# Optimization experiments

Measured on AMD Instinct MI355X. Metric: run time of the kernel, lower is better.

Reference implementation:

```python
import jax, jax.numpy as jnp
import numpy as np

D, H, HS, L, V, B, T = 384, 8, 48, 8, 32000, 32, 128
EPS = 1e-5


def setup_inputs() -> dict:
    key = jax.random.key(0)
    ks = jax.random.split(key, 10)
    s = 0.02
    return {
        'index': jax.random.randint(ks[0], (B, T), 0, V),
        'tok_emb': jax.random.normal(ks[1], (V, D), jnp.float32) * s,
        'pos_emb': jax.random.normal(ks[2], (V, D), jnp.float32) * s,
        'Wq': jax.random.normal(ks[3], (L, D, D), jnp.float32) * s,
        'Wk': jax.random.normal(ks[4], (L, D, D), jnp.float32) * s,
        'Wv': jax.random.normal(ks[5], (L, D, D), jnp.float32) * s,
        'Wo': jax.random.normal(ks[6], (L, D, D), jnp.float32) * s,
        'bo': jnp.zeros((L, D), jnp.float32),
        'W1': jax.random.normal(ks[7], (L, D, 4 * D), jnp.float32) * s,
        'b1': jnp.zeros((L, 4 * D), jnp.float32),
        'W2': jax.random.normal(ks[8], (L, 4 * D, D), jnp.float32) * s,
        'b2': jnp.zeros((L, D), jnp.float32),
        'ln1g': jnp.ones((L, D), jnp.float32),
        'ln1b': jnp.zeros((L, D), jnp.float32),
        'ln2g': jnp.ones((L, D), jnp.float32),
        'ln2b': jnp.zeros((L, D), jnp.float32),
        'lnfg': jnp.ones((D,), jnp.float32),
        'lnfb': jnp.zeros((D,), jnp.float32),
        'lmW': jax.random.normal(ks[9], (D, V), jnp.float32) * s,
        'lmb': jnp.zeros((V,), jnp.float32),
    }


def _layer_norm(x, g, b):
    m = jnp.mean(x, axis=-1, keepdims=True)
    xc = x - m
    v = jnp.mean(xc * xc, axis=-1, keepdims=True)
    return xc * jax.lax.rsqrt(v + EPS) * g + b


def _forward(index, tok_emb, pos_emb, Wq, Wk, Wv, Wo, bo, W1, b1, W2, b2,
             ln1g, ln1b, ln2g, ln2b, lnfg, lnfb, lmW, lmb):
    Bx, Tx = index.shape
    x = tok_emb[index] + pos_emb[jnp.arange(Tx)]  # [B,T,D]
    tril = jnp.tril(jnp.ones((Tx, Tx), bool))
    scale = HS ** -0.5
    neg_inf = jnp.finfo(x.dtype).min
    for l in range(L):
        q = (x @ Wq[l]).reshape(Bx, Tx, H, HS)
        k = (x @ Wk[l]).reshape(Bx, Tx, H, HS)
        v = (x @ Wv[l]).reshape(Bx, Tx, H, HS)
        wei = jnp.einsum('bthd,bshd->bhts', q, k) * scale  # [B,H,T,T]
        wei = jnp.where(tril, wei, neg_inf)
        wei = jax.nn.softmax(wei, axis=-1)
        attn = jnp.einsum('bhts,bshd->bthd', wei, v).reshape(Bx, Tx, D)
        y = attn @ Wo[l] + bo[l]
        x = _layer_norm(x + y, ln1g[l], ln1b[l])  # post-LN as in source
        y = jax.nn.relu(x @ W1[l] + b1[l]) @ W2[l] + b2[l]
        x = _layer_norm(x + y, ln2g[l], ln2b[l])
    x = _layer_norm(x, lnfg, lnfb)
    logits = x @ lmW + lmb  # [B,T,V]
    return logits


def reference(index, tok_emb, pos_emb, Wq, Wk, Wv, Wo, bo, W1, b1, W2, b2,
              ln1g, ln1b, ln2g, ln2b, lnfg, lnfb, lmW, lmb):
    return _forward(index, tok_emb, pos_emb, Wq, Wk, Wv, Wo, bo, W1, b1, W2,
                    b2, ln1g, ln1b, ln2g, ln2b, lnfg, lnfb, lmW, lmb)
```

## Files before the change

### kernel.cpp

```cpp
#include <hip/hip_runtime.h>
#include <cstdint>
#include <cstddef>

#define D_  384
#define H_  8
#define HS_ 48
#define L_  8
#define V_  32000
#define B_  32
#define T_  128
#define M_  4096

typedef __bf16 bf16;
typedef __bf16 bf16x8 __attribute__((ext_vector_type(8)));
typedef float  floatx4 __attribute__((ext_vector_type(4)));

__device__ __forceinline__ unsigned short bfbits(float f) {
  union { bf16 b; unsigned short u; } cv; cv.b = (bf16)f; return cv.u;
}
__device__ __forceinline__ float bflo(unsigned u) {
  union { float f; unsigned x; } c; c.x = u << 16; return c.f;
}
__device__ __forceinline__ float bfhi(unsigned u) {
  union { float f; unsigned x; } c; c.x = u & 0xffff0000u; return c.f;
}

__device__ __forceinline__ float waveReduceSum(float v) {
  #pragma unroll
  for (int off = 32; off > 0; off >>= 1) v += __shfl_xor(v, off, 64);
  return v;
}

__global__ void embed_kernel(const int* __restrict__ idx, const float* __restrict__ tok,
                             const float* __restrict__ pos, float* __restrict__ x,
                             bf16* __restrict__ xb) {
  int e = blockIdx.x * 256 + threadIdx.x;
  int row = e / 96, c4 = (e % 96) * 4;
  int t = row & (T_ - 1);
  int tk = idx[row];
  const float4 tv = *(const float4*)(tok + (size_t)tk * D_ + c4);
  const float4 pv = *(const float4*)(pos + (size_t)t * D_ + c4);
  float4 o; o.x = tv.x + pv.x; o.y = tv.y + pv.y; o.z = tv.z + pv.z; o.w = tv.w + pv.w;
  *(float4*)(x + (size_t)row * D_ + c4) = o;
  uint2 u;
  u.x = (unsigned)bfbits(o.x) | ((unsigned)bfbits(o.y) << 16);
  u.y = (unsigned)bfbits(o.z) | ((unsigned)bfbits(o.w) << 16);
  *(uint2*)(xb + (size_t)row * D_ + c4) = u;
}

__device__ __forceinline__ void transpose_tile(const float* __restrict__ src, bf16* __restrict__ dst,
                                               int K, int N, int k0, int n0) {
  __shared__ float tile[32][33];
  const int r = threadIdx.x >> 5, c = threadIdx.x & 31;
  #pragma unroll
  for (int i = 0; i < 4; i++)
    tile[r + 8*i][c] = src[(size_t)(k0 + r + 8*i) * N + n0 + c];
  __syncthreads();
  #pragma unroll
  for (int i = 0; i < 4; i++)
    dst[(size_t)(n0 + r + 8*i) * K + k0 + c] = (bf16)tile[c][r + 8*i];
}

__global__ __launch_bounds__(256) void t_layer_kernel(
    const float* __restrict__ Wq, const float* __restrict__ Wk,
    const float* __restrict__ Wv, const float* __restrict__ Wo,
    const float* __restrict__ W1, const float* __restrict__ W2,
    bf16* __restrict__ wqkvoT, bf16* __restrict__ w1t, bf16* __restrict__ w2t) {
  if (blockIdx.z == 0) {
    const int mm = blockIdx.x / 12, nx = blockIdx.x % 12;
    const float* src = mm == 0 ? Wq : mm == 1 ? Wk : mm == 2 ? Wv : Wo;
    transpose_tile(src, wqkvoT + (size_t)mm * (D_ * D_), D_, D_, blockIdx.y * 32, nx * 32);
  } else if (blockIdx.z == 1) {
    transpose_tile(W1, w1t, D_, 4 * D_, blockIdx.y * 32, blockIdx.x * 32);
  } else {
    transpose_tile(W2, w2t, 4 * D_, D_, blockIdx.x * 32, blockIdx.y * 32);
  }
}

__global__ __launch_bounds__(256) void t_head_kernel(const float* __restrict__ lmW, bf16* __restrict__ dst) {
  transpose_tile(lmW, dst, D_, V_, blockIdx.y * 32, blockIdx.x * 32);
}

template<bool BIAS, bool RESID, bool RELU, bool OUTBF>
__device__ __forceinline__ void gemm_core(
    const bf16* __restrict__ A, const bf16* __restrict__ Bt,
    const float* __restrict__ bias, const float* __restrict__ resid,
    void* __restrict__ Cout, int N, int K, int m0, int n0)
{
  __shared__ bf16 As[128][56];
  __shared__ bf16 Bs[128][56];
  const int tid  = threadIdx.x;
  const int lane = tid & 63;
  const int wave = tid >> 6;
  const int wr = wave >> 1, wc = wave & 1;
  const int lrow = lane & 15, quad = lane >> 4;

  floatx4 acc[4][4];
  #pragma unroll
  for (int i = 0; i < 4; i++)
    #pragma unroll
    for (int j = 0; j < 4; j++) acc[i][j] = floatx4{0.f, 0.f, 0.f, 0.f};

  const int r0 = tid >> 2,          p0 = (tid & 3) * 8;
  const int r1 = (tid + 256) >> 2,  p1 = p0;

  for (int k0 = 0; k0 < K; k0 += 32) {
    __syncthreads();
    const uint4 a0 = *(const uint4*)(A  + (size_t)(m0 + r0) * K + k0 + p0);
    const uint4 a1 = *(const uint4*)(A  + (size_t)(m0 + r1) * K + k0 + p1);
    const uint4 b0 = *(const uint4*)(Bt + (size_t)(n0 + r0) * K + k0 + p0);
    const uint4 b1 = *(const uint4*)(Bt + (size_t)(n0 + r1) * K + k0 + p1);
    *(uint4*)&As[r0][p0] = a0;
    *(uint4*)&As[r1][p1] = a1;
    *(uint4*)&Bs[r0][p0] = b0;
    *(uint4*)&Bs[r1][p1] = b1;
    __syncthreads();
    bf16x8 af[4], bfr[4];
    #pragma unroll
    for (int mt = 0; mt < 4; mt++) af[mt]  = *(const bf16x8*)&As[wr*64 + mt*16 + lrow][quad*8];
    #pragma unroll
    for (int nt = 0; nt < 4; nt++) bfr[nt] = *(const bf16x8*)&Bs[wc*64 + nt*16 + lrow][quad*8];
    #pragma unroll
    for (int mt = 0; mt < 4; mt++)
      #pragma unroll
      for (int nt = 0; nt < 4; nt++)
        acc[mt][nt] = __builtin_amdgcn_mfma_f32_16x16x32_bf16(af[mt], bfr[nt], acc[mt][nt], 0, 0, 0);
  }

  #pragma unroll
  for (int mt = 0; mt < 4; mt++) {
    #pragma unroll
    for (int nt = 0; nt < 4; nt++) {
      const int col = n0 + wc*64 + nt*16 + lrow;
      float bv = 0.f;
      if (BIAS) bv = bias[col];
      #pragma unroll
      for (int i = 0; i < 4; i++) {
        const int row = m0 + wr*64 + mt*16 + quad*4 + i;
        float vv = acc[mt][nt][i] + bv;
        if (RESID) vv += resid[(size_t)row * N + col];
        if (RELU)  vv = vv > 0.f ? vv : 0.f;
        if (OUTBF) ((bf16*)Cout)[(size_t)row * N + col] = (bf16)vv;
        else       ((float*)Cout)[(size_t)row * N + col] = vv;
      }
    }
  }
}

template<bool BIAS, bool RESID, bool RELU, bool OUTBF>
__global__ __launch_bounds__(256) void gemm_kernel(const bf16* __restrict__ A, const bf16* __restrict__ Bt,
    const float* __restrict__ bias, const float* __restrict__ resid, void* __restrict__ C, int N, int K) {
  gemm_core<BIAS, RESID, RELU, OUTBF>(A, Bt, bias, resid, C, N, K, blockIdx.x * 128, blockIdx.y * 128);
}

__global__ __launch_bounds__(256) void gemm_qkv_kernel(const bf16* __restrict__ A, const bf16* __restrict__ Wt,
    bf16* __restrict__ q, bf16* __restrict__ k, bf16* __restrict__ v) {
  const bf16* Bt = Wt + (size_t)blockIdx.z * (D_ * D_);
  bf16* C = blockIdx.z == 0 ? q : (blockIdx.z == 1 ? k : v);
  gemm_core<false, false, false, true>(A, Bt, nullptr, nullptr, C, D_, D_, blockIdx.x * 128, blockIdx.y * 128);
}

__global__ __launch_bounds__(512) void attn_kernel(const bf16* __restrict__ q,
    const bf16* __restrict__ k, const bf16* __restrict__ v, bf16* __restrict__ attnb) {
  __shared__ float ks[T_][48];
  __shared__ float vs[T_][48];
  const int bh = blockIdx.x;
  const int b = bh >> 3, h = bh & 7;
  const int r  = threadIdx.x >> 2;
  const int qq = threadIdx.x & 3;
  const int o  = qq * 12;
  const size_t rowbase = ((size_t)(b * T_ + r)) * D_ + h * HS_ + o;
  float qr[12];
  #pragma unroll
  for (int j = 0; j < 3; j++) {
    const uint2 tk = *(const uint2*)(k + rowbase + 4*j);
    const uint2 tv = *(const uint2*)(v + rowbase + 4*j);
    const uint2 tq = *(const uint2*)(q + rowbase + 4*j);
    float4 fk, fv;
    fk.x = bflo(tk.x); fk.y = bfhi(tk.x); fk.z = bflo(tk.y); fk.w = bfhi(tk.y);
    fv.x = bflo(tv.x); fv.y = bfhi(tv.x); fv.z = bflo(tv.y); fv.w = bfhi(tv.y);
    *(float4*)&ks[r][o + 4*j] = fk;
    *(float4*)&vs[r][o + 4*j] = fv;
    qr[4*j]   = bflo(tq.x); qr[4*j+1] = bfhi(tq.x);
    qr[4*j+2] = bflo(tq.y); qr[4*j+3] = bfhi(tq.y);
  }
  __syncthreads();
  float m = -3.0e38f, l = 0.f, acc[12];
  #pragma unroll
  for (int j = 0; j < 12; j++) acc[j] = 0.f;
  const float scale = 0.14433756729740643f;
  for (int c = 0; c < T_; c++) {
    float s = 0.f;
    #pragma unroll
    for (int j = 0; j < 12; j++) s += qr[j] * ks[c][o + j];
    s += __shfl_xor(s, 1, 64);
    s += __shfl_xor(s, 2, 64);
    s *= scale;
    if (c > r) s = -3.0e38f;
    const float mn = fmaxf(m, s);
    const float al = __expf(m - mn);
    const float pp = __expf(s - mn);
    l = l * al + pp;
    #pragma unroll
    for (int j = 0; j < 12; j++) acc[j] = acc[j] * al + pp * vs[c][o + j];
    m = mn;
  }
  const float inv = 1.f / l;
  unsigned ob[6];
  #pragma unroll
  for (int j = 0; j < 6; j++)
    ob[j] = (unsigned)bfbits(acc[2*j] * inv) | ((unsigned)bfbits(acc[2*j+1] * inv) << 16);
  bf16* dst = attnb + rowbase;
  #pragma unroll
  for (int j = 0; j < 3; j++) {
    uint2 u; u.x = ob[2*j]; u.y = ob[2*j+1];
    *(uint2*)(dst + 4*j) = u;
  }
}

__global__ __launch_bounds__(256) void ln_kernel(const float* __restrict__ in,
    const float* __restrict__ g, const float* __restrict__ bta,
    float* __restrict__ xo, bf16* __restrict__ xbo) {
  const int wave = threadIdx.x >> 6, lane = threadIdx.x & 63;
  const int row = blockIdx.x * 4 + wave;
  const float* p = in + (size_t)row * D_;
  float v[6];
  #pragma unroll
  for (int j = 0; j < 6; j++) v[j] = p[lane + 64*j];
  float s = 0.f;
  #pragma unroll
  for (int j = 0; j < 6; j++) s += v[j];
  s = waveReduceSum(s);
  const float mean = s * (1.f / 384.f);
  float qv = 0.f;
  #pragma unroll
  for (int j = 0; j < 6; j++) { v[j] -= mean; qv += v[j] * v[j]; }
  qv = waveReduceSum(qv);
  const float rs = rsqrtf(qv * (1.f / 384.f) + 1e-5f);
  #pragma unroll
  for (int j = 0; j < 6; j++) {
    const int c = lane + 64*j;
    const float o = v[j] * rs * g[c] + bta[c];
    xo[(size_t)row * D_ + c]  = o;
    xbo[(size_t)row * D_ + c] = (bf16)o;
  }
}

extern "C" void kernel_launch(void* const* d_in, const int* in_sizes, int n_in,
                              void* d_out, int out_size, void* d_ws, size_t ws_size,
                              hipStream_t stream) {
  const int*   index = (const int*)  d_in[0];
  const float* tok   = (const float*)d_in[1];
  const float* pos   = (const float*)d_in[2];
  const float* Wq    = (const float*)d_in[3];
  const float* Wk    = (const float*)d_in[4];
  const float* Wv    = (const float*)d_in[5];
  const float* Wo    = (const float*)d_in[6];
  const float* bo    = (const float*)d_in[7];
  const float* W1    = (const float*)d_in[8];
  const float* b1    = (const float*)d_in[9];
  const float* W2    = (const float*)d_in[10];
  const float* b2    = (const float*)d_in[11];
  const float* ln1g  = (const float*)d_in[12];
  const float* ln1b  = (const float*)d_in[13];
  const float* ln2g  = (const float*)d_in[14];
  const float* ln2b  = (const float*)d_in[15];
  const float* lnfg  = (const float*)d_in[16];
  const float* lnfb  = (const float*)d_in[17];
  const float* lmW   = (const float*)d_in[18];
  const float* lmb   = (const float*)d_in[19];
  float* out = (float*)d_out;
  char* ws = (char*)d_ws;

  float* x     = (float*)(ws + 0);
  float* tmp   = (float*)(ws + 6291456);
  bf16*  xb    = (bf16*) (ws + 12582912);
  bf16*  qb    = (bf16*) (ws + 15728640);
  bf16*  kb    = (bf16*) (ws + 18874368);
  bf16*  vb    = (bf16*) (ws + 22020096);
  bf16*  attnb = (bf16*) (ws + 25165824);
  bf16*  hb    = (bf16*) (ws + 28311552);
  bf16*  wqkvoT= (bf16*) (ws + 40894464);
  bf16*  w1t   = (bf16*) (ws + 42074112);
  bf16*  w2t   = (bf16*) (ws + 43253760);
  bf16*  lmT   = (bf16*) (ws + 15728640);

  embed_kernel<<<1536, 256, 0, stream>>>(index, tok, pos, x, xb);
  for (int l = 0; l < L_; l++) {
    t_layer_kernel<<<dim3(48, 12, 3), 256, 0, stream>>>(
        Wq + (size_t)l * D_ * D_, Wk + (size_t)l * D_ * D_,
        Wv + (size_t)l * D_ * D_, Wo + (size_t)l * D_ * D_,
        W1 + (size_t)l * D_ * 4 * D_, W2 + (size_t)l * 4 * D_ * D_,
        wqkvoT, w1t, w2t);
    gemm_qkv_kernel<<<dim3(32, 3, 3), 256, 0, stream>>>(xb, wqkvoT, qb, kb, vb);
    attn_kernel<<<256, 512, 0, stream>>>(qb, kb, vb, attnb);
    gemm_kernel<true, true, false, false><<<dim3(32, 3), 256, 0, stream>>>(
        attnb, wqkvoT + 3 * D_ * D_, bo + l * D_, x, tmp, D_, D_);
    ln_kernel<<<1024, 256, 0, stream>>>(tmp, ln1g + l * D_, ln1b + l * D_, x, xb);
    gemm_kernel<true, false, true, true><<<dim3(32, 12), 256, 0, stream>>>(
        xb, w1t, b1 + l * 4 * D_, nullptr, hb, 4 * D_, D_);
    gemm_kernel<true, true, false, false><<<dim3(32, 3), 256, 0, stream>>>(
        hb, w2t, b2 + l * D_, x, tmp, D_, 4 * D_);
    ln_kernel<<<1024, 256, 0, stream>>>(tmp, ln2g + l * D_, ln2b + l * D_, x, xb);
  }
  ln_kernel<<<1024, 256, 0, stream>>>(x, lnfg, lnfb, x, xb);
  t_head_kernel<<<dim3(1000, 12), 256, 0, stream>>>(lmW, lmT);
  gemm_kernel<true, false, false, false><<<dim3(32, 250), 256, 0, stream>>>(
      xb, lmT, lmb, nullptr, out, V_, D_);
}
```

Measured before the change: 1.799 ms.

## Use direct global-to-LDS loads with XOR swizzle and 64-row tiles for N=384 GEMMs

The GEMM core now loads A and B tiles straight from global memory into LDS with global_load_lds, skipping the register round-trip. The LDS tiles drop their padding and use an XOR-swizzled column layout to avoid bank conflicts. The block M size becomes a template parameter, and the Wo and W2 projections switch to 64-row tiles so their launches have twice as many blocks. The main loop still uses two barriers per k-step and no double buffering, so load latency is not overlapped with the MFMA work.

```diff
diff --git a/kernel.cpp b/kernel.cpp
--- a/kernel.cpp
+++ b/kernel.cpp
@@ -29,6 +29,12 @@
   #pragma unroll
   for (int off = 32; off > 0; off >>= 1) v += __shfl_xor(v, off, 64);
   return v;
+}
+
+__device__ __forceinline__ void gload_lds16(const void* g, void* l) {
+  __builtin_amdgcn_global_load_lds(
+      (const __attribute__((address_space(1))) void*)g,
+      (__attribute__((address_space(3))) void*)l, 16, 0, 0);
 }
 
 __global__ void embed_kernel(const int* __restrict__ idx, const float* __restrict__ tok,
@@ -81,62 +87,69 @@
   transpose_tile(lmW, dst, D_, V_, blockIdx.y * 32, blockIdx.x * 32);
 }
 
-template<bool BIAS, bool RESID, bool RELU, bool OUTBF>
+template<int BM, bool BIAS, bool RESID, bool RELU, bool OUTBF>
 __device__ __forceinline__ void gemm_core(
     const bf16* __restrict__ A, const bf16* __restrict__ Bt,
     const float* __restrict__ bias, const float* __restrict__ resid,
     void* __restrict__ Cout, int N, int K, int m0, int n0)
 {
-  __shared__ bf16 As[128][56];
-  __shared__ bf16 Bs[128][56];
+  constexpr int MTC = BM / 32;
+  __shared__ bf16 As[BM * 32];
+  __shared__ bf16 Bs[128 * 32];
   const int tid  = threadIdx.x;
   const int lane = tid & 63;
   const int wave = tid >> 6;
   const int wr = wave >> 1, wc = wave & 1;
   const int lrow = lane & 15, quad = lane >> 4;
-
-  floatx4 acc[4][4];
-  #pragma unroll
-  for (int i = 0; i < 4; i++)
+  const int rdoff = ((quad ^ ((lrow >> 1) & 3)) << 3);
+
+  const int srow = lane >> 2;
+  const int scol = (((lane & 3) ^ ((lane >> 3) & 3)) << 3);
+
+  floatx4 acc[MTC][4];
+  #pragma unroll
+  for (int i = 0; i < MTC; i++)
     #pragma unroll
     for (int j = 0; j < 4; j++) acc[i][j] = floatx4{0.f, 0.f, 0.f, 0.f};
 
-  const int r0 = tid >> 2,          p0 = (tid & 3) * 8;
-  const int r1 = (tid + 256) >> 2,  p1 = p0;
+  const bf16* gA = A  + (size_t)(m0 + wave * (BM / 4) + srow) * K + scol;
+  const bf16* gB = Bt + (size_t)(n0 + wave * 32       + srow) * K + scol;
+  bf16* lA = As + wave * (BM * 8);
+  bf16* lB = Bs + wave * 1024;
 
   for (int k0 = 0; k0 < K; k0 += 32) {
+    #pragma unroll
+    for (int j = 0; j < BM / 64; j++)
+      gload_lds16(gA + k0 + (size_t)j * 16 * K, lA + j * 512);
+    #pragma unroll
+    for (int j = 0; j < 2; j++)
+      gload_lds16(gB + k0 + (size_t)j * 16 * K, lB + j * 512);
     __syncthreads();
-    const uint4 a0 = *(const uint4*)(A  + (size_t)(m0 + r0) * K + k0 + p0);
-    const uint4 a1 = *(const uint4*)(A  + (size_t)(m0 + r1) * K + k0 + p1);
-    const uint4 b0 = *(const uint4*)(Bt + (size_t)(n0 + r0) * K + k0 + p0);
-    const uint4 b1 = *(const uint4*)(Bt + (size_t)(n0 + r1) * K + k0 + p1);
-    *(uint4*)&As[r0][p0] = a0;
-    *(uint4*)&As[r1][p1] = a1;
-    *(uint4*)&Bs[r0][p0] = b0;
-    *(uint4*)&Bs[r1][p1] = b1;
-    __syncthreads();
-    bf16x8 af[4], bfr[4];
-    #pragma unroll
-    for (int mt = 0; mt < 4; mt++) af[mt]  = *(const bf16x8*)&As[wr*64 + mt*16 + lrow][quad*8];
-    #pragma unroll
-    for (int nt = 0; nt < 4; nt++) bfr[nt] = *(const bf16x8*)&Bs[wc*64 + nt*16 + lrow][quad*8];
-    #pragma unroll
-    for (int mt = 0; mt < 4; mt++)
+    bf16x8 af[MTC], bfr[4];
+    #pragma unroll
+    for (int mt = 0; mt < MTC; mt++)
+      af[mt]  = *(const bf16x8*)&As[(wr * (BM / 2) + mt * 16 + lrow) * 32 + rdoff];
+    #pragma unroll
+    for (int nt = 0; nt < 4; nt++)
+      bfr[nt] = *(const bf16x8*)&Bs[(wc * 64 + nt * 16 + lrow) * 32 + rdoff];
+    #pragma unroll
+    for (int mt = 0; mt < MTC; mt++)
       #pragma unroll
       for (int nt = 0; nt < 4; nt++)
         acc[mt][nt] = __builtin_amdgcn_mfma_f32_16x16x32_bf16(af[mt], bfr[nt], acc[mt][nt], 0, 0, 0);
-  }
-
-  #pragma unroll
-  for (int mt = 0; mt < 4; mt++) {
+    __syncthreads();
+  }
+
+  #pragma unroll
+  for (int mt = 0; mt < MTC; mt++) {
     #pragma unroll
     for (int nt = 0; nt < 4; nt++) {
-      const int col = n0 + wc*64 + nt*16 + lrow;
+      const int col = n0 + wc * 64 + nt * 16 + lrow;
       float bv = 0.f;
       if (BIAS) bv = bias[col];
       #pragma unroll
       for (int i = 0; i < 4; i++) {
-        const int row = m0 + wr*64 + mt*16 + quad*4 + i;
+        const int row = m0 + wr * (BM / 2) + mt * 16 + quad * 4 + i;
         float vv = acc[mt][nt][i] + bv;
         if (RESID) vv += resid[(size_t)row * N + col];
         if (RELU)  vv = vv > 0.f ? vv : 0.f;
@@ -147,17 +160,17 @@
   }
 }
 
-template<bool BIAS, bool RESID, bool RELU, bool OUTBF>
+template<int BM, bool BIAS, bool RESID, bool RELU, bool OUTBF>
 __global__ __launch_bounds__(256) void gemm_kernel(const bf16* __restrict__ A, const bf16* __restrict__ Bt,
     const float* __restrict__ bias, const float* __restrict__ resid, void* __restrict__ C, int N, int K) {
-  gemm_core<BIAS, RESID, RELU, OUTBF>(A, Bt, bias, resid, C, N, K, blockIdx.x * 128, blockIdx.y * 128);
+  gemm_core<BM, BIAS, RESID, RELU, OUTBF>(A, Bt, bias, resid, C, N, K, blockIdx.x * BM, blockIdx.y * 128);
 }
 
 __global__ __launch_bounds__(256) void gemm_qkv_kernel(const bf16* __restrict__ A, const bf16* __restrict__ Wt,
     bf16* __restrict__ q, bf16* __restrict__ k, bf16* __restrict__ v) {
   const bf16* Bt = Wt + (size_t)blockIdx.z * (D_ * D_);
   bf16* C = blockIdx.z == 0 ? q : (blockIdx.z == 1 ? k : v);
-  gemm_core<false, false, false, true>(A, Bt, nullptr, nullptr, C, D_, D_, blockIdx.x * 128, blockIdx.y * 128);
+  gemm_core<128, false, false, false, true>(A, Bt, nullptr, nullptr, C, D_, D_, blockIdx.x * 128, blockIdx.y * 128);
 }
 
 __global__ __launch_bounds__(512) void attn_kernel(const bf16* __restrict__ q,
@@ -294,17 +307,17 @@
         wqkvoT, w1t, w2t);
     gemm_qkv_kernel<<<dim3(32, 3, 3), 256, 0, stream>>>(xb, wqkvoT, qb, kb, vb);
     attn_kernel<<<256, 512, 0, stream>>>(qb, kb, vb, attnb);
-    gemm_kernel<true, true, false, false><<<dim3(32, 3), 256, 0, stream>>>(
+    gemm_kernel<64, true, true, false, false><<<dim3(64, 3), 256, 0, stream>>>(
         attnb, wqkvoT + 3 * D_ * D_, bo + l * D_, x, tmp, D_, D_);
     ln_kernel<<<1024, 256, 0, stream>>>(tmp, ln1g + l * D_, ln1b + l * D_, x, xb);
-    gemm_kernel<true, false, true, true><<<dim3(32, 12), 256, 0, stream>>>(
+    gemm_kernel<128, true, false, true, true><<<dim3(32, 12), 256, 0, stream>>>(
         xb, w1t, b1 + l * 4 * D_, nullptr, hb, 4 * D_, D_);
-    gemm_kernel<true, true, false, false><<<dim3(32, 3), 256, 0, stream>>>(
+    gemm_kernel<64, true, true, false, false><<<dim3(64, 3), 256, 0, stream>>>(
         hb, w2t, b2 + l * D_, x, tmp, D_, 4 * D_);
     ln_kernel<<<1024, 256, 0, stream>>>(tmp, ln2g + l * D_, ln2b + l * D_, x, xb);
   }
   ln_kernel<<<1024, 256, 0, stream>>>(x, lnfg, lnfb, x, xb);
   t_head_kernel<<<dim3(1000, 12), 256, 0, stream>>>(lmW, lmT);
-  gemm_kernel<true, false, false, false><<<dim3(32, 250), 256, 0, stream>>>(
+  gemm_kernel<128, true, false, false, false><<<dim3(32, 250), 256, 0, stream>>>(
       xb, lmT, lmb, nullptr, out, V_, D_);
 }
```

New measurement: 1.655 ms. 8.0% less time.
